# Kernel tuning notes

Measured on AMD Instinct MI355X. Metric: run time of the kernel, lower is better.

## Reference

```python
import jax, jax.numpy as jnp
import numpy as np

EMBED_DIM = 1024
NUM_HEADS = 16
HEAD_DIM = EMBED_DIM // NUM_HEADS  # 64
SCALING = 0.125
T, B = 2048, 2


def setup_inputs() -> dict:
    key = jax.random.key(0)
    k_q, k_len, k_w1, k_b1, k_w2, k_b2 = jax.random.split(key, 6)
    query = jax.random.normal(k_q, (T, B, EMBED_DIM), dtype=jnp.float32)
    # realistic padding: each sequence has a valid length in [T//2, T)
    lengths = jax.random.randint(k_len, (B,), T // 2, T)
    key_padding_mask = jnp.arange(T)[None, :] >= lengths[:, None]  # [B, T] bool, True = pad
    s1 = 1.0 / np.sqrt(EMBED_DIM)
    W_in = jax.random.uniform(k_w1, (3 * EMBED_DIM, EMBED_DIM), jnp.float32, -s1, s1)
    b_in = jax.random.uniform(k_b1, (3 * EMBED_DIM,), jnp.float32, -s1, s1)
    W_out = jax.random.uniform(k_w2, (EMBED_DIM, EMBED_DIM), jnp.float32, -s1, s1)
    b_out = jax.random.uniform(k_b2, (EMBED_DIM,), jnp.float32, -s1, s1)
    return {"query": query, "key_padding_mask": key_padding_mask,
            "W_in": W_in, "b_in": b_in, "W_out": W_out, "b_out": b_out}


def reference(query, key_padding_mask, W_in, b_in, W_out, b_out):
    # query: [T, B, E]; key_padding_mask: [B, S] bool (True = padded key)
    t, b, e = query.shape
    h, hd = NUM_HEADS, HEAD_DIM
    proj = query @ W_in.T + b_in                      # [T, B, 3E]
    q, k, v = jnp.split(proj, 3, axis=-1)             # each [T, B, E]
    q = q * SCALING

    def to_bh(x):  # [T, B, E] -> [B*H, T, hd], matching torch view+transpose
        return x.reshape(t, b * h, hd).transpose(1, 0, 2)

    q, k, v = to_bh(q), to_bh(k), to_bh(v)
    attn_weights = jnp.einsum('bth,bsh->bts', q, k)   # [B*H, T, S]
    attn_weights = attn_weights.reshape(b, h, t, t)
    attn_weights = jnp.where(key_padding_mask[:, None, None, :], -jnp.inf, attn_weights)
    # softmax computed in float32 then cast back, as in the original
    attn_weights = jax.nn.softmax(attn_weights.astype(jnp.float32), axis=-1).astype(query.dtype)
    # dropout p=0 (eval/inference) -> identity
    attn = jnp.einsum('bhts,bhsd->bhtd', attn_weights, v.reshape(b, h, t, hd))  # [B,H,T,hd]
    attn = attn.reshape(b * h, t, hd).transpose(1, 0, 2).reshape(t, b, e)       # [T,B,E]
    return attn @ W_out.T + b_out
```

## Files before the change

kernel.cpp:

```cpp
#include <hip/hip_runtime.h>
#include <hip/hip_bf16.h>
#include <stdint.h>
#include <stddef.h>

typedef __hip_bfloat16 bf16;
typedef __attribute__((ext_vector_type(4))) float f32x4;
typedef __attribute__((ext_vector_type(8))) short s16x8;
typedef __attribute__((ext_vector_type(4))) short s16x4;

#define AS1 __attribute__((address_space(1)))
#define AS3 __attribute__((address_space(3)))

__device__ __forceinline__ void async_ld16(const void* g, void* l) {
  __builtin_amdgcn_global_load_lds((AS1 void*)g, (AS3 void*)l, 16, 0, 0);
}

#if __has_builtin(__builtin_amdgcn_exp2f)
#define EXP2F(x) __builtin_amdgcn_exp2f(x)
#else
#define EXP2F(x) exp2f(x)
#endif

__device__ __forceinline__ unsigned pk_bf16(float a, float b) {
  unsigned ua = __builtin_bit_cast(unsigned, a);
  unsigned ub = __builtin_bit_cast(unsigned, b);
  ua += 0x7FFFu + ((ua >> 16) & 1u);
  ub += 0x7FFFu + ((ub >> 16) & 1u);
  return (ua >> 16) | (ub & 0xFFFF0000u);
}

__device__ __forceinline__ unsigned pk_trunc(float a, float b) {
  return __builtin_amdgcn_perm(__builtin_bit_cast(unsigned, b),
                               __builtin_bit_cast(unsigned, a), 0x07060302u);
}

__global__ __launch_bounds__(256) void convert_all_kernel(const float* __restrict__ q_src,
                                                          const float* __restrict__ wi_src,
                                                          const float* __restrict__ wo_src,
                                                          bf16* __restrict__ q_dst,
                                                          bf16* __restrict__ wi_dst,
                                                          bf16* __restrict__ wo_dst,
                                                          const void* __restrict__ mask,
                                                          int* __restrict__ lengths) {
  int blk = blockIdx.x;
  if (blk >= 4096) {
    __shared__ int s_any;
    __shared__ int s_cnt[256];
    const int tid = threadIdx.x;
    const int b = blk - 4096;
    const unsigned char* m8 = (const unsigned char*)mask;
    if (tid == 0) s_any = 0;
    __syncthreads();
    int local = 0;
    for (int i = tid; i < 4096; i += 256) local |= m8[i];
    if (local) atomicOr(&s_any, 1);
    __syncthreads();
    int cnt = 0;
    if (s_any) {
      for (int t = tid; t < 2048; t += 256) cnt += (m8[b * 2048 + t] == 0) ? 1 : 0;
    } else {
      const int* m32 = (const int*)mask;
      for (int t = tid; t < 2048; t += 256) cnt += (m32[b * 2048 + t] == 0) ? 1 : 0;
    }
    s_cnt[tid] = cnt;
    __syncthreads();
    for (int s = 128; s > 0; s >>= 1) {
      if (tid < s) s_cnt[tid] += s_cnt[tid + s];
      __syncthreads();
    }
    if (tid == 0) lengths[b] = s_cnt[0];
    return;
  }
  const float* src;
  bf16* dst;
  int base;
  if (blk < 2048)      { src = q_src;  dst = q_dst;  base = blk * 2048; }
  else if (blk < 3584) { src = wi_src; dst = wi_dst; base = (blk - 2048) * 2048; }
  else                 { src = wo_src; dst = wo_dst; base = (blk - 3584) * 2048; }
  int i = base + threadIdx.x * 8;
  float4 a = *(const float4*)(src + i);
  float4 b = *(const float4*)(src + i + 4);
  unsigned u[4];
  u[0] = pk_bf16(a.x, a.y); u[1] = pk_bf16(a.z, a.w);
  u[2] = pk_bf16(b.x, b.y); u[3] = pk_bf16(b.z, b.w);
  *(uint4*)(dst + i) = *(const uint4*)u;
}

__device__ __forceinline__ void gemm_mainloop(const bf16* __restrict__ A,
                                              const bf16* __restrict__ Bm,
                                              bf16* As, bf16* Bs,
                                              int m0, int n0, f32x4 (&acc)[4][4]) {
  const int K = 1024;
  const int tid = threadIdx.x;
  const int wave = tid >> 6, lane = tid & 63;
  const int col = lane & 15, quad = lane >> 4;
  const int wm = wave & 1, wn = wave >> 1;
#pragma unroll
  for (int mi = 0; mi < 4; mi++)
#pragma unroll
    for (int ni = 0; ni < 4; ni++) acc[mi][ni] = (f32x4){0.f, 0.f, 0.f, 0.f};

  const int c0 = wave * 128 + lane;
  const int rowA0 = c0 >> 2, kc0 = (c0 & 3) * 8;
  const int c1 = c0 + 64;
  const int rowA1 = c1 >> 2, kc1 = (c1 & 3) * 8;
  char* ldsA0 = (char*)As + (size_t)(wave * 128) * 16;
  char* ldsA1 = ldsA0 + 64 * 16;
  char* ldsB0 = (char*)Bs + (size_t)(wave * 128) * 16;
  char* ldsB1 = ldsB0 + 64 * 16;
  const bf16* gA0 = A + (size_t)(m0 + rowA0) * K + kc0;
  const bf16* gA1 = A + (size_t)(m0 + rowA1) * K + kc1;
  const bf16* gB0 = Bm + (size_t)(n0 + rowA0) * K + kc0;
  const bf16* gB1 = Bm + (size_t)(n0 + rowA1) * K + kc1;

  for (int k0 = 0; k0 < K; k0 += 32) {
    async_ld16(gA0 + k0, ldsA0);
    async_ld16(gA1 + k0, ldsA1);
    async_ld16(gB0 + k0, ldsB0);
    async_ld16(gB1 + k0, ldsB1);
    __syncthreads();
    s16x8 af[4], bfr[4];
#pragma unroll
    for (int mi = 0; mi < 4; mi++)
      af[mi] = *(const s16x8*)(As + (wm * 64 + mi * 16 + col) * 32 + quad * 8);
#pragma unroll
    for (int ni = 0; ni < 4; ni++)
      bfr[ni] = *(const s16x8*)(Bs + (wn * 64 + ni * 16 + col) * 32 + quad * 8);
#pragma unroll
    for (int mi = 0; mi < 4; mi++)
#pragma unroll
      for (int ni = 0; ni < 4; ni++)
        acc[mi][ni] = __builtin_amdgcn_mfma_f32_16x16x32_bf16(af[mi], bfr[ni], acc[mi][ni], 0, 0, 0);
    __syncthreads();
  }
}

__global__ __launch_bounds__(256) void gemm_qkv(const bf16* __restrict__ X,
                                                const bf16* __restrict__ W,
                                                const float* __restrict__ bias,
                                                bf16* __restrict__ Qd,
                                                bf16* __restrict__ Kd,
                                                bf16* __restrict__ Vt) {
  __shared__ bf16 As[128 * 32];
  __shared__ bf16 Bs[128 * 32];
  const int m0 = blockIdx.y * 128, n0 = blockIdx.x * 128;
  f32x4 acc[4][4];
  gemm_mainloop(X, W, As, Bs, m0, n0, acc);
  const int tid = threadIdx.x;
  const int wave = tid >> 6, lane = tid & 63;
  const int col = lane & 15, quad = lane >> 4;
  const int wm = wave & 1, wn = wave >> 1;
  const float QSCALE = 0.125f * 1.4426950408889634f;
#pragma unroll
  for (int mi = 0; mi < 4; mi++)
#pragma unroll
    for (int ni = 0; ni < 4; ni++)
#pragma unroll
      for (int r = 0; r < 4; r++) {
        int m = m0 + wm * 64 + mi * 16 + quad * 4 + r;
        int n = n0 + wn * 64 + ni * 16 + col;
        float v = acc[mi][ni][r] + bias[n];
        int e = n & 1023, hh = e >> 6, d = e & 63;
        int t = m >> 1, b = m & 1;
        int bh = b * 16 + hh;
        if (n < 1024) {
          Qd[((size_t)bh * 2048 + t) * 64 + d] = __float2bfloat16(v * QSCALE);
        } else if (n < 2048) {
          Kd[((size_t)bh * 2048 + t) * 64 + d] = __float2bfloat16(v);
        } else {
          int sl = t & 63;
          int perm = ((sl >> 2) & 3) * 16 + (sl >> 4) * 4 + (sl & 3);
          Vt[(size_t)bh * 131072 + (t >> 6) * 4096 + d * 64 + perm] = __float2bfloat16(v);
        }
      }
}

__global__ __launch_bounds__(512, 4) void attn_kernel(const bf16* __restrict__ Qd,
                                                      const bf16* __restrict__ Kd,
                                                      const bf16* __restrict__ Vt,
                                                      const int* __restrict__ lengths,
                                                      bf16* __restrict__ attn_out) {
  __shared__ bf16 Ks[2][2][64 * 64];
  __shared__ bf16 Vs[2][2][64 * 64];

  const int id = blockIdx.x;
  const int slot = id >> 3;
  const int bh = (id & 7) * 4 + (slot & 3);
  const int qt0 = (slot >> 2) * 128;
  const int b = bh >> 4, h = bh & 15;

  const int tid = threadIdx.x;
  const int wave = tid >> 6, lane = tid & 63;
  const int half = wave >> 2, hw = wave & 3;
  const int col = lane & 15, quad = lane >> 4;
  const int len = lengths[b];
  const int nfull = len >> 6;
  const int rem = len & 63;
  const int nkt = nfull + (rem ? 1 : 0);
  const int nh0 = (nkt + 1) >> 1;
  const int first = half ? nh0 : 0;
  const int cnt = half ? (nkt - nh0) : nh0;

  s16x8 bq[2][2];
#pragma unroll
  for (int g = 0; g < 2; g++) {
    const bf16* qptr =
        Qd + ((size_t)bh * 2048 + qt0 + hw * 32 + g * 16 + col) * 64 + quad * 8;
    bq[g][0] = *(const s16x8*)(qptr);
    bq[g][1] = *(const s16x8*)(qptr + 32);
  }

  const int kbase0 = col * 128 + ((quad ^ (col & 7)) << 4);
  const int kbase1 = kbase0 ^ 64;
  const int vbase0 = col * 128 + (((quad << 1) ^ (col & 7)) << 4);
  const int vbase1 = vbase0 ^ 16;
  const int HBUF = half * 16384;

  const bf16* Kg = Kd + (size_t)bh * 2048 * 64;
  const bf16* Vg = Vt + (size_t)bh * 131072;
  const int c0 = hw * 128 + lane, c1 = c0 + 64;
  const int r0 = c0 >> 3, j0 = (c0 & 7) ^ (r0 & 7);
  const int r1 = c1 >> 3, j1 = (c1 & 7) ^ (r1 & 7);
  const bf16* gK0 = Kg + r0 * 64 + j0 * 8;
  const bf16* gK1 = Kg + r1 * 64 + j1 * 8;
  const bf16* gV0 = Vg + r0 * 64 + j0 * 8;
  const bf16* gV1 = Vg + r1 * 64 + j1 * 8;
  const int dst0 = (hw * 128) * 16, dst1 = (hw * 128 + 64) * 16;

  auto stage = [&](int kt, int BUF) {
    const int off = kt * 4096;
    async_ld16(gK0 + off, (char*)Ks + BUF + dst0);
    async_ld16(gK1 + off, (char*)Ks + BUF + dst1);
    async_ld16(gV0 + off, (char*)Vs + BUF + dst0);
    async_ld16(gV1 + off, (char*)Vs + BUF + dst1);
  };

  const s16x4 aOnes = {0x3F80, 0x3F80, 0x3F80, 0x3F80};
  const f32x4 Zf = (f32x4){0.f, 0.f, 0.f, 0.f};
  f32x4 lacc[2] = {Zf, Zf};
  f32x4 oaccT[2][4];
#pragma unroll
  for (int g = 0; g < 2; g++)
#pragma unroll
    for (int dt = 0; dt < 4; dt++) oaccT[g][dt] = Zf;

  auto score = [&](int BUF, f32x4 (&s0)[4], f32x4 (&s1)[4]) {
#pragma unroll
    for (int ti = 0; ti < 4; ti++) {
      const s16x8 ak0 = *(const s16x8*)((char*)Ks + BUF + ti * 2048 + kbase0);
      s0[ti] = __builtin_amdgcn_mfma_f32_16x16x32_bf16(ak0, bq[0][0], Zf, 0, 0, 0);
      s1[ti] = __builtin_amdgcn_mfma_f32_16x16x32_bf16(ak0, bq[1][0], Zf, 0, 0, 0);
      const s16x8 ak1 = *(const s16x8*)((char*)Ks + BUF + ti * 2048 + kbase1);
      s0[ti] = __builtin_amdgcn_mfma_f32_16x16x32_bf16(ak1, bq[0][1], s0[ti], 0, 0, 0);
      s1[ti] = __builtin_amdgcn_mfma_f32_16x16x32_bf16(ak1, bq[1][1], s1[ti], 0, 0, 0);
    }
  };
  auto accum = [&](int BUF, s16x4 (&bP0)[4], s16x4 (&bP1)[4]) {
#pragma unroll
    for (int ti = 0; ti < 4; ti++) {
      lacc[0] = __builtin_amdgcn_mfma_f32_16x16x16bf16_1k(aOnes, bP0[ti], lacc[0], 0, 0, 0);
      lacc[1] = __builtin_amdgcn_mfma_f32_16x16x16bf16_1k(aOnes, bP1[ti], lacc[1], 0, 0, 0);
    }
#pragma unroll
    for (int dt = 0; dt < 4; dt++) {
#pragma unroll
      for (int sh = 0; sh < 2; sh++) {
        const s16x8 av = *(const s16x8*)((char*)Vs + BUF + dt * 2048 + (sh ? vbase1 : vbase0));
        const s16x4 alo = __builtin_shufflevector(av, av, 0, 1, 2, 3);
        const s16x4 ahi = __builtin_shufflevector(av, av, 4, 5, 6, 7);
        oaccT[0][dt] = __builtin_amdgcn_mfma_f32_16x16x16bf16_1k(alo, bP0[sh * 2], oaccT[0][dt], 0, 0, 0);
        oaccT[0][dt] = __builtin_amdgcn_mfma_f32_16x16x16bf16_1k(ahi, bP0[sh * 2 + 1], oaccT[0][dt], 0, 0, 0);
        oaccT[1][dt] = __builtin_amdgcn_mfma_f32_16x16x16bf16_1k(alo, bP1[sh * 2], oaccT[1][dt], 0, 0, 0);
        oaccT[1][dt] = __builtin_amdgcn_mfma_f32_16x16x16bf16_1k(ahi, bP1[sh * 2 + 1], oaccT[1][dt], 0, 0, 0);
      }
    }
  };

  auto tile_full = [&](int BUF) {
    f32x4 s0[4], s1[4];
    score(BUF, s0, s1);
    s16x4 bP0[4], bP1[4];
#pragma unroll
    for (int ti = 0; ti < 4; ti++) {
      uint2 u0 = {pk_trunc(EXP2F(s0[ti][0]), EXP2F(s0[ti][1])),
                  pk_trunc(EXP2F(s0[ti][2]), EXP2F(s0[ti][3]))};
      bP0[ti] = __builtin_bit_cast(s16x4, u0);
      uint2 u1 = {pk_trunc(EXP2F(s1[ti][0]), EXP2F(s1[ti][1])),
                  pk_trunc(EXP2F(s1[ti][2]), EXP2F(s1[ti][3]))};
      bP1[ti] = __builtin_bit_cast(s16x4, u1);
    }
    accum(BUF, bP0, bP1);
  };

  auto tile_mask = [&](int BUF) {
    f32x4 s0[4], s1[4];
    score(BUF, s0, s1);
    s16x4 bP0[4], bP1[4];
#pragma unroll
    for (int ti = 0; ti < 4; ti++) {
      const int sb = ti * 16 + quad * 4;
      float a0 = (sb + 0 < rem) ? EXP2F(s0[ti][0]) : 0.f;
      float a1 = (sb + 1 < rem) ? EXP2F(s0[ti][1]) : 0.f;
      float a2 = (sb + 2 < rem) ? EXP2F(s0[ti][2]) : 0.f;
      float a3 = (sb + 3 < rem) ? EXP2F(s0[ti][3]) : 0.f;
      uint2 u0 = {pk_trunc(a0, a1), pk_trunc(a2, a3)};
      bP0[ti] = __builtin_bit_cast(s16x4, u0);
      float c0m = (sb + 0 < rem) ? EXP2F(s1[ti][0]) : 0.f;
      float c1m = (sb + 1 < rem) ? EXP2F(s1[ti][1]) : 0.f;
      float c2m = (sb + 2 < rem) ? EXP2F(s1[ti][2]) : 0.f;
      float c3m = (sb + 3 < rem) ? EXP2F(s1[ti][3]) : 0.f;
      uint2 u1 = {pk_trunc(c0m, c1m), pk_trunc(c2m, c3m)};
      bP1[ti] = __builtin_bit_cast(s16x4, u1);
    }
    accum(BUF, bP0, bP1);
  };

  stage(first, HBUF);
  __syncthreads();
  for (int i = 0; i < nh0; i++) {
    if (i + 1 < cnt) stage(first + i + 1, HBUF + ((i + 1) & 1) * 8192);
    if (i < cnt) {
      const int kt = first + i;
      const int BUF = HBUF + (i & 1) * 8192;
      if (kt < nfull) tile_full(BUF); else tile_mask(BUF);
    }
    __syncthreads();
  }

  float* OF = (float*)Ks;
  float* LF = (float*)Vs;
  const int me = hw * 64 + lane;
  if (half == 1) {
#pragma unroll
    for (int g = 0; g < 2; g++) {
      LF[g * 256 + me] = lacc[g][0];
#pragma unroll
      for (int dt = 0; dt < 4; dt++)
#pragma unroll
        for (int r = 0; r < 4; r++)
          OF[(g * 16 + dt * 4 + r) * 256 + me] = oaccT[g][dt][r];
    }
  }
  __syncthreads();
  if (half == 0) {
#pragma unroll
    for (int g = 0; g < 2; g++) {
      const float linv = 1.0f / (lacc[g][0] + LF[g * 256 + me]);
      const int t = qt0 + hw * 32 + g * 16 + col;
      bf16* outp = attn_out + ((size_t)t * 2 + b) * 1024 + h * 64 + quad * 4;
#pragma unroll
      for (int dt = 0; dt < 4; dt++) {
        float o0 = (oaccT[g][dt][0] + OF[(g * 16 + dt * 4 + 0) * 256 + me]) * linv;
        float o1 = (oaccT[g][dt][1] + OF[(g * 16 + dt * 4 + 1) * 256 + me]) * linv;
        float o2 = (oaccT[g][dt][2] + OF[(g * 16 + dt * 4 + 2) * 256 + me]) * linv;
        float o3 = (oaccT[g][dt][3] + OF[(g * 16 + dt * 4 + 3) * 256 + me]) * linv;
        uint2 u = {pk_bf16(o0, o1), pk_bf16(o2, o3)};
        *(uint2*)(outp + dt * 16) = u;
      }
    }
  }
}

__global__ __launch_bounds__(256) void gemm_out(const bf16* __restrict__ Aa,
                                                const bf16* __restrict__ W,
                                                const float* __restrict__ bias,
                                                float* __restrict__ out) {
  __shared__ bf16 Bs[128 * 64];
  __shared__ bf16 As[64 * 64];
  const int K = 1024;
  const int m0 = blockIdx.y * 64, n0 = blockIdx.x * 128;
  const int tid = threadIdx.x;
  const int wave = tid >> 6, lane = tid & 63;
  const int col = lane & 15, quad = lane >> 4;

  f32x4 acc[8];
#pragma unroll
  for (int ni = 0; ni < 8; ni++) acc[ni] = (f32x4){0.f, 0.f, 0.f, 0.f};

  const bf16* gB[4];
  char* ldsB[4];
#pragma unroll
  for (int i = 0; i < 4; i++) {
    const int c = tid + 256 * i;
    gB[i] = W + (size_t)(n0 + (c >> 3)) * K + (c & 7) * 8;
    ldsB[i] = (char*)Bs + (size_t)(wave * 64 + 256 * i) * 16;
  }
  const bf16* gA[2];
  char* ldsA[2];
#pragma unroll
  for (int i = 0; i < 2; i++) {
    const int c = tid + 256 * i;
    gA[i] = Aa + (size_t)(m0 + (c >> 3)) * K + (c & 7) * 8;
    ldsA[i] = (char*)As + (size_t)(wave * 64 + 256 * i) * 16;
  }

  for (int k0 = 0; k0 < K; k0 += 64) {
#pragma unroll
    for (int i = 0; i < 4; i++) async_ld16(gB[i] + k0, ldsB[i]);
#pragma unroll
    for (int i = 0; i < 2; i++) async_ld16(gA[i] + k0, ldsA[i]);
    __syncthreads();
    const s16x8 af0 = *(const s16x8*)(As + (wave * 16 + col) * 64 + quad * 8);
    const s16x8 af1 = *(const s16x8*)(As + (wave * 16 + col) * 64 + 32 + quad * 8);
#pragma unroll
    for (int ni = 0; ni < 8; ni++) {
      const s16x8 b0 = *(const s16x8*)(Bs + (ni * 16 + col) * 64 + quad * 8);
      acc[ni] = __builtin_amdgcn_mfma_f32_16x16x32_bf16(af0, b0, acc[ni], 0, 0, 0);
      const s16x8 b1 = *(const s16x8*)(Bs + (ni * 16 + col) * 64 + 32 + quad * 8);
      acc[ni] = __builtin_amdgcn_mfma_f32_16x16x32_bf16(af1, b1, acc[ni], 0, 0, 0);
    }
    __syncthreads();
  }

#pragma unroll
  for (int ni = 0; ni < 8; ni++)
#pragma unroll
    for (int r = 0; r < 4; r++) {
      int m = m0 + wave * 16 + quad * 4 + r;
      int n = n0 + ni * 16 + col;
      out[(size_t)m * 1024 + n] = acc[ni][r] + bias[n];
    }
}

extern "C" void kernel_launch(void* const* d_in, const int* in_sizes, int n_in,
                              void* d_out, int out_size, void* d_ws, size_t ws_size,
                              hipStream_t stream) {
  (void)in_sizes; (void)n_in; (void)out_size; (void)ws_size;
  const float* query = (const float*)d_in[0];
  const void*  mask  = d_in[1];
  const float* W_in  = (const float*)d_in[2];
  const float* b_in  = (const float*)d_in[3];
  const float* W_out = (const float*)d_in[4];
  const float* b_out = (const float*)d_in[5];
  float* out = (float*)d_out;

  char* ws = (char*)d_ws;
  bf16* Xbf    = (bf16*)(ws);
  bf16* attnb  = (bf16*)(ws);
  bf16* Winbf  = (bf16*)(ws + 8388608);
  bf16* Woutbf = (bf16*)(ws + 8388608 + 6291456);
  bf16* Qd     = (bf16*)(ws + 16777216);
  bf16* Kd     = (bf16*)(ws + 25165824);
  bf16* Vt     = (bf16*)(ws + 33554432);
  int*  lens   = (int*)(ws + 41943040);

  convert_all_kernel<<<4098, 256, 0, stream>>>(query, W_in, W_out, Xbf, Winbf, Woutbf,
                                               mask, lens);
  gemm_qkv<<<dim3(24, 32), 256, 0, stream>>>(Xbf, Winbf, b_in, Qd, Kd, Vt);
  attn_kernel<<<512, 512, 0, stream>>>(Qd, Kd, Vt, lens, attnb);
  gemm_out<<<dim3(8, 64), 256, 0, stream>>>(attnb, Woutbf, b_out, out);
}
```

Baseline: 196.0 us.

## Restructure QKV GEMM with K=64 swizzled LDS, XCD-aware tiling, staged V store

The QKV GEMM now loads 64-wide K slices per barrier instead of 32, which halves the number of sync points. Its LDS uses an XOR swizzle to avoid bank conflicts, and the launch is remapped to a 1D grid so each XCD owns a contiguous set of N tiles to improve L2 reuse of weights. The V-tile epilogue is staged through LDS as packed bf16 pairs, so the permuted transposed layout is written with coalesced 16-byte stores instead of scattered 2-byte ones. The output GEMM gets the same LDS swizzle. LDS use per block doubles, which may lower occupancy.

```diff
diff --git a/kernel.cpp b/kernel.cpp
--- a/kernel.cpp
+++ b/kernel.cpp
@@ -86,93 +86,125 @@
   *(uint4*)(dst + i) = *(const uint4*)u;
 }
 
-__device__ __forceinline__ void gemm_mainloop(const bf16* __restrict__ A,
-                                              const bf16* __restrict__ Bm,
-                                              bf16* As, bf16* Bs,
-                                              int m0, int n0, f32x4 (&acc)[4][4]) {
-  const int K = 1024;
-  const int tid = threadIdx.x;
-  const int wave = tid >> 6, lane = tid & 63;
-  const int col = lane & 15, quad = lane >> 4;
-  const int wm = wave & 1, wn = wave >> 1;
-#pragma unroll
-  for (int mi = 0; mi < 4; mi++)
-#pragma unroll
-    for (int ni = 0; ni < 4; ni++) acc[mi][ni] = (f32x4){0.f, 0.f, 0.f, 0.f};
-
-  const int c0 = wave * 128 + lane;
-  const int rowA0 = c0 >> 2, kc0 = (c0 & 3) * 8;
-  const int c1 = c0 + 64;
-  const int rowA1 = c1 >> 2, kc1 = (c1 & 3) * 8;
-  char* ldsA0 = (char*)As + (size_t)(wave * 128) * 16;
-  char* ldsA1 = ldsA0 + 64 * 16;
-  char* ldsB0 = (char*)Bs + (size_t)(wave * 128) * 16;
-  char* ldsB1 = ldsB0 + 64 * 16;
-  const bf16* gA0 = A + (size_t)(m0 + rowA0) * K + kc0;
-  const bf16* gA1 = A + (size_t)(m0 + rowA1) * K + kc1;
-  const bf16* gB0 = Bm + (size_t)(n0 + rowA0) * K + kc0;
-  const bf16* gB1 = Bm + (size_t)(n0 + rowA1) * K + kc1;
-
-  for (int k0 = 0; k0 < K; k0 += 32) {
-    async_ld16(gA0 + k0, ldsA0);
-    async_ld16(gA1 + k0, ldsA1);
-    async_ld16(gB0 + k0, ldsB0);
-    async_ld16(gB1 + k0, ldsB1);
-    __syncthreads();
-    s16x8 af[4], bfr[4];
-#pragma unroll
-    for (int mi = 0; mi < 4; mi++)
-      af[mi] = *(const s16x8*)(As + (wm * 64 + mi * 16 + col) * 32 + quad * 8);
-#pragma unroll
-    for (int ni = 0; ni < 4; ni++)
-      bfr[ni] = *(const s16x8*)(Bs + (wn * 64 + ni * 16 + col) * 32 + quad * 8);
-#pragma unroll
-    for (int mi = 0; mi < 4; mi++)
-#pragma unroll
-      for (int ni = 0; ni < 4; ni++)
-        acc[mi][ni] = __builtin_amdgcn_mfma_f32_16x16x32_bf16(af[mi], bfr[ni], acc[mi][ni], 0, 0, 0);
-    __syncthreads();
-  }
-}
-
 __global__ __launch_bounds__(256) void gemm_qkv(const bf16* __restrict__ X,
                                                 const bf16* __restrict__ W,
                                                 const float* __restrict__ bias,
                                                 bf16* __restrict__ Qd,
                                                 bf16* __restrict__ Kd,
                                                 bf16* __restrict__ Vt) {
-  __shared__ bf16 As[128 * 32];
-  __shared__ bf16 Bs[128 * 32];
-  const int m0 = blockIdx.y * 128, n0 = blockIdx.x * 128;
-  f32x4 acc[4][4];
-  gemm_mainloop(X, W, As, Bs, m0, n0, acc);
+  __shared__ bf16 smem[128 * 64 * 2];
+  bf16* As = smem;
+  bf16* Bs = smem + 8192;
+  const int K = 1024;
+  const int id = blockIdx.x;
+  const int xcd = id & 7;
+  const int local = id >> 3;
+  const int nloc = local % 3;
+  const int by = local / 3;
+  const int m0 = by * 128;
+  const int n0 = (xcd * 3 + nloc) * 128;
   const int tid = threadIdx.x;
   const int wave = tid >> 6, lane = tid & 63;
   const int col = lane & 15, quad = lane >> 4;
   const int wm = wave & 1, wn = wave >> 1;
+
+  f32x4 acc[4][4];
+#pragma unroll
+  for (int mi = 0; mi < 4; mi++)
+#pragma unroll
+    for (int ni = 0; ni < 4; ni++) acc[mi][ni] = (f32x4){0.f, 0.f, 0.f, 0.f};
+
+  const bf16* gA[4];
+  const bf16* gB[4];
+  char* ldA[4];
+  char* ldB[4];
+#pragma unroll
+  for (int i = 0; i < 4; i++) {
+    const int c = tid + 256 * i;
+    const int row = c >> 3;
+    const int j = (c & 7) ^ (row & 7);
+    gA[i] = X + (size_t)(m0 + row) * K + j * 8;
+    gB[i] = W + (size_t)(n0 + row) * K + j * 8;
+    ldA[i] = (char*)As + (size_t)(wave * 64 + 256 * i) * 16;
+    ldB[i] = (char*)Bs + (size_t)(wave * 64 + 256 * i) * 16;
+  }
+
+  for (int k0 = 0; k0 < K; k0 += 64) {
+#pragma unroll
+    for (int i = 0; i < 4; i++) async_ld16(gA[i] + k0, ldA[i]);
+#pragma unroll
+    for (int i = 0; i < 4; i++) async_ld16(gB[i] + k0, ldB[i]);
+    __syncthreads();
+#pragma unroll
+    for (int kh = 0; kh < 2; kh++) {
+      s16x8 af[4], bfr[4];
+#pragma unroll
+      for (int mi = 0; mi < 4; mi++) {
+        const int row = wm * 64 + mi * 16 + col;
+        af[mi] = *(const s16x8*)((char*)As + row * 128 + (((kh << 2) | quad) ^ (row & 7)) * 16);
+      }
+#pragma unroll
+      for (int ni = 0; ni < 4; ni++) {
+        const int row = wn * 64 + ni * 16 + col;
+        bfr[ni] = *(const s16x8*)((char*)Bs + row * 128 + (((kh << 2) | quad) ^ (row & 7)) * 16);
+      }
+#pragma unroll
+      for (int mi = 0; mi < 4; mi++)
+#pragma unroll
+        for (int ni = 0; ni < 4; ni++)
+          acc[mi][ni] = __builtin_amdgcn_mfma_f32_16x16x32_bf16(af[mi], bfr[ni], acc[mi][ni], 0, 0, 0);
+    }
+    __syncthreads();
+  }
+
   const float QSCALE = 0.125f * 1.4426950408889634f;
-#pragma unroll
-  for (int mi = 0; mi < 4; mi++)
-#pragma unroll
-    for (int ni = 0; ni < 4; ni++)
-#pragma unroll
-      for (int r = 0; r < 4; r++) {
-        int m = m0 + wm * 64 + mi * 16 + quad * 4 + r;
-        int n = n0 + wn * 64 + ni * 16 + col;
-        float v = acc[mi][ni][r] + bias[n];
-        int e = n & 1023, hh = e >> 6, d = e & 63;
-        int t = m >> 1, b = m & 1;
-        int bh = b * 16 + hh;
-        if (n < 1024) {
-          Qd[((size_t)bh * 2048 + t) * 64 + d] = __float2bfloat16(v * QSCALE);
-        } else if (n < 2048) {
-          Kd[((size_t)bh * 2048 + t) * 64 + d] = __float2bfloat16(v);
-        } else {
-          int sl = t & 63;
-          int perm = ((sl >> 2) & 3) * 16 + (sl >> 4) * 4 + (sl & 3);
-          Vt[(size_t)bh * 131072 + (t >> 6) * 4096 + d * 64 + perm] = __float2bfloat16(v);
+  if (n0 < 2048) {
+    bf16* dstb = (n0 < 1024) ? Qd : Kd;
+    const float sc = (n0 < 1024) ? QSCALE : 1.0f;
+#pragma unroll
+    for (int mi = 0; mi < 4; mi++)
+#pragma unroll
+      for (int ni = 0; ni < 4; ni++)
+#pragma unroll
+        for (int r = 0; r < 4; r++) {
+          int m = m0 + wm * 64 + mi * 16 + quad * 4 + r;
+          int n = n0 + wn * 64 + ni * 16 + col;
+          float v = (acc[mi][ni][r] + bias[n]) * sc;
+          int e = n & 1023, hh = e >> 6, d = e & 63;
+          int t = m >> 1, b = m & 1;
+          int bh = b * 16 + hh;
+          dstb[((size_t)bh * 2048 + t) * 64 + d] = __float2bfloat16(v);
+        }
+  } else {
+    const int hh0 = (n0 - 2048) >> 6;
+#pragma unroll
+    for (int mi = 0; mi < 4; mi++) {
+      const int s0i = wm * 32 + mi * 8 + quad * 2;
+      const int perm0 = ((s0i >> 2) & 3) * 16 + (s0i >> 4) * 4 + (s0i & 3);
+#pragma unroll
+      for (int ni = 0; ni < 4; ni++) {
+        const int n = n0 + wn * 64 + ni * 16 + col;
+        const float bv = bias[n];
+        const int d = ni * 16 + col;
+#pragma unroll
+        for (int b = 0; b < 2; b++) {
+          float v0 = acc[mi][ni][b] + bv;
+          float v1 = acc[mi][ni][b + 2] + bv;
+          const int p = b * 2 + wn;
+          *(unsigned*)((char*)smem + (p * 4096 + d * 64 + perm0) * 2) = pk_bf16(v0, v1);
         }
       }
+    }
+    __syncthreads();
+    const int bh = (wave >> 1) * 16 + hh0 + (wave & 1);
+    bf16* dstp = Vt + (size_t)bh * 131072 + (m0 >> 7) * 4096;
+    const char* srcp = (const char*)smem + wave * 8192;
+#pragma unroll
+    for (int j = 0; j < 8; j++) {
+      s16x8 v = *(const s16x8*)(srcp + j * 1024 + lane * 16);
+      *(s16x8*)(dstp + j * 512 + lane * 8) = v;
+    }
+  }
 }
 
 __global__ __launch_bounds__(512, 4) void attn_kernel(const bf16* __restrict__ Qd,
@@ -382,7 +414,9 @@
 #pragma unroll
   for (int i = 0; i < 4; i++) {
     const int c = tid + 256 * i;
-    gB[i] = W + (size_t)(n0 + (c >> 3)) * K + (c & 7) * 8;
+    const int row = c >> 3;
+    const int j = (c & 7) ^ (row & 7);
+    gB[i] = W + (size_t)(n0 + row) * K + j * 8;
     ldsB[i] = (char*)Bs + (size_t)(wave * 64 + 256 * i) * 16;
   }
   const bf16* gA[2];
@@ -390,7 +424,9 @@
 #pragma unroll
   for (int i = 0; i < 2; i++) {
     const int c = tid + 256 * i;
-    gA[i] = Aa + (size_t)(m0 + (c >> 3)) * K + (c & 7) * 8;
+    const int row = c >> 3;
+    const int j = (c & 7) ^ (row & 7);
+    gA[i] = Aa + (size_t)(m0 + row) * K + j * 8;
     ldsA[i] = (char*)As + (size_t)(wave * 64 + 256 * i) * 16;
   }
 
@@ -400,13 +436,17 @@
 #pragma unroll
     for (int i = 0; i < 2; i++) async_ld16(gA[i] + k0, ldsA[i]);
     __syncthreads();
-    const s16x8 af0 = *(const s16x8*)(As + (wave * 16 + col) * 64 + quad * 8);
-    const s16x8 af1 = *(const s16x8*)(As + (wave * 16 + col) * 64 + 32 + quad * 8);
+    const int arow = wave * 16 + col;
+    const int abase = arow * 128 + ((quad ^ (arow & 7)) << 4);
+    const s16x8 af0 = *(const s16x8*)((char*)As + abase);
+    const s16x8 af1 = *(const s16x8*)((char*)As + (abase ^ 64));
 #pragma unroll
     for (int ni = 0; ni < 8; ni++) {
-      const s16x8 b0 = *(const s16x8*)(Bs + (ni * 16 + col) * 64 + quad * 8);
+      const int brow = ni * 16 + col;
+      const int bbase = brow * 128 + ((quad ^ (brow & 7)) << 4);
+      const s16x8 b0 = *(const s16x8*)((char*)Bs + bbase);
       acc[ni] = __builtin_amdgcn_mfma_f32_16x16x32_bf16(af0, b0, acc[ni], 0, 0, 0);
-      const s16x8 b1 = *(const s16x8*)(Bs + (ni * 16 + col) * 64 + 32 + quad * 8);
+      const s16x8 b1 = *(const s16x8*)((char*)Bs + (bbase ^ 64));
       acc[ni] = __builtin_amdgcn_mfma_f32_16x16x32_bf16(af1, b1, acc[ni], 0, 0, 0);
     }
     __syncthreads();
@@ -446,7 +486,7 @@
 
   convert_all_kernel<<<4098, 256, 0, stream>>>(query, W_in, W_out, Xbf, Winbf, Woutbf,
                                                mask, lens);
-  gemm_qkv<<<dim3(24, 32), 256, 0, stream>>>(Xbf, Winbf, b_in, Qd, Kd, Vt);
+  gemm_qkv<<<768, 256, 0, stream>>>(Xbf, Winbf, b_in, Qd, Kd, Vt);
   attn_kernel<<<512, 512, 0, stream>>>(Qd, Kd, Vt, lens, attnb);
   gemm_out<<<dim3(8, 64), 256, 0, stream>>>(attnb, Woutbf, b_out, out);
 }
```

Result: faster. 189.3 us (-3.4%).
